# Performance work log

Measured on AMD Instinct MI355X. Metric: run time of the kernel, lower is better.

The kernel has to match this reference:

```python
import jax, jax.numpy as jnp
import numpy as np

B, T = 64, 4096
K = 67            # 25 body + 21 + 21 hand keypoints
D = 256           # first_layer_size
C = 7             # num_classes
THR = 0.1         # confidence_threshold
EPS = 1e-5        # BatchNorm eps


def setup_inputs() -> dict:
    key = jax.random.key(0)
    ks = jax.random.split(key, 8)
    body = jax.random.normal(ks[0], (B, T, 75), dtype=jnp.float32)
    hand_right = jax.random.normal(ks[1], (B, T, 63), dtype=jnp.float32)
    hand_left = jax.random.normal(ks[2], (B, T, 63), dtype=jnp.float32)
    length = jax.random.randint(ks[3], (B,), 1, T + 1, dtype=jnp.int64)
    W1 = jax.random.normal(ks[4], (2 * K, D), dtype=jnp.float32) * 0.05
    b1 = jnp.zeros((D,), dtype=jnp.float32)
    gamma = jnp.ones((D,), dtype=jnp.float32)
    beta = jnp.zeros((D,), dtype=jnp.float32)
    Wc = jax.random.normal(ks[5], (D, C), dtype=jnp.float32) * 0.05
    bc = jnp.zeros((C,), dtype=jnp.float32)
    return {"body": body, "hand_right": hand_right, "hand_left": hand_left,
            "length": length, "W1": W1, "b1": b1, "gamma": gamma,
            "beta": beta, "Wc": Wc, "bc": bc}


def reference(body, hand_right, hand_left, length, W1, b1, gamma, beta, Wc, bc):
    # concat keypoint streams -> [B, T, 3K] -> [B, T, K, 3]
    feats = jnp.concatenate([body, hand_right, hand_left], axis=2)
    feats = feats.reshape(feats.shape[0], feats.shape[1], -1, 3)
    x, y, conf = feats[..., 0], feats[..., 1], feats[..., 2]
    conf = (conf > THR).astype(feats.dtype)
    # gate coords by confidence, flatten to [B, T, 2K]
    pos = jnp.stack([x * conf, y * conf], axis=3)
    pos = pos.reshape(pos.shape[0], pos.shape[1], -1)
    # static MLP: Linear + ReLU -> [B, T, D]
    sf = jax.nn.relu(jnp.einsum("btf,fd->btd", pos, W1) + b1)
    # masked max pool over valid timesteps (vectorized segment-max)
    mask = jnp.arange(sf.shape[1])[None, :] < length[:, None]      # [B, T]
    pooled = jnp.max(jnp.where(mask[:, :, None], sf, -jnp.inf), axis=1)  # [B, D]
    # BatchNorm1d (training mode: batch statistics)
    mean = pooled.mean(axis=0)
    var = pooled.var(axis=0)
    bn = (pooled - mean) / jnp.sqrt(var + EPS) * gamma + beta
    # classifier
    return bn @ Wc + bc
```

## Files before the change

### kernel.cpp

```cpp
#include <hip/hip_runtime.h>
#include <hip/hip_bf16.h>

#define B_   64
#define T_   4096
#define K_   67
#define F_   134
#define FP_  160
#define D_   256
#define C_   7
#define THR_ 0.1f
#define EPS_ 1e-5f

typedef __bf16 bf16x8 __attribute__((ext_vector_type(8)));
typedef float  f32x4  __attribute__((ext_vector_type(4)));


__device__ __forceinline__ int a_idx(int t, int f) {
    return (((t >> 4) * 5 + (f >> 5)) * 512) +
           ((((f >> 3) & 3) * 16 + (t & 15)) * 8) + (f & 7);
}

__device__ __forceinline__ int get_len(const int* L, int b) {
    return (L[1] == 0) ? L[2 * b] : L[b];
}

__global__ void convert_w1(const float* __restrict__ W1, __bf16* __restrict__ W1bf) {
    int idx = blockIdx.x * 256 + threadIdx.x;
    if (idx >= D_ * FP_) return;
    int d = idx / FP_, f = idx - d * FP_;
    float v = (f < F_) ? W1[f * D_ + d] : 0.f;
    W1bf[idx] = (__bf16)v;
}

__device__ __forceinline__ void stage_triple(const float* p, int t, int kglob,
                                             __bf16* As) {
    float x = p[0], y = p[1], cf = p[2];
    if (!(cf > THR_)) { x = 0.f; y = 0.f; }
    unsigned short ux = __builtin_bit_cast(unsigned short, (__bf16)x);
    unsigned short uy = __builtin_bit_cast(unsigned short, (__bf16)y);
    int idx = a_idx(t, 2 * kglob);
    *(unsigned int*)((unsigned short*)As + idx) =
        (unsigned int)ux | ((unsigned int)uy << 16);
}

__global__ __launch_bounds__(256, 2)
void fused_mlp_pool(const float* __restrict__ body,
                    const float* __restrict__ hr,
                    const float* __restrict__ hl,
                    const int*   __restrict__ length,
                    const float* __restrict__ b1,
                    const __bf16* __restrict__ W1bf,
                    float* __restrict__ pooled)
{
    const int b = blockIdx.y;
    const int len = get_len(length, b);
    const int t0 = blockIdx.x * 64;
    if (t0 >= len) return;

    __shared__ __align__(16) __bf16 As[4 * 5 * 512];

    const int tid  = threadIdx.x;
    const int wave = tid >> 6;
    const int lane = tid & 63;
    const int quad = lane >> 4;
    const int l16  = lane & 15;
    const int dbase = wave * 64;

    bf16x8 bfrag[4][5];
    float  b1v[4];
#pragma unroll
    for (int n = 0; n < 4; n++) {
        int d = dbase + n * 16 + l16;
        const __bf16* p = W1bf + d * FP_ + quad * 8;
#pragma unroll
        for (int kt = 0; kt < 5; kt++)
            bfrag[n][kt] = *(const bf16x8*)(p + kt * 32);
        b1v[n] = b1[d];
    }

    for (int i = tid; i < 64 * 13; i += 256) {
        int t = i / 13;
        int f = 134 + 2 * (i % 13);
        *(unsigned int*)((unsigned short*)As + a_idx(t, f)) = 0u;
    }

    const long rowb = (long)b * T_;
    const float* bodyt = body + (rowb + t0) * 75;
    for (int j = tid; j < 64 * 25; j += 256) {
        int t = j / 25, k = j - t * 25;
        stage_triple(bodyt + t * 75 + k * 3, t, k, As);
    }
    const float* hrt = hr + (rowb + t0) * 63;
    for (int j = tid; j < 64 * 21; j += 256) {
        int t = j / 21, k = j - t * 21;
        stage_triple(hrt + t * 63 + k * 3, t, 25 + k, As);
    }
    const float* hlt = hl + (rowb + t0) * 63;
    for (int j = tid; j < 64 * 21; j += 256) {
        int t = j / 21, k = j - t * 21;
        stage_triple(hlt + t * 63 + k * 3, t, 46 + k, As);
    }
    __syncthreads();

    f32x4 acc[4][4];
#pragma unroll
    for (int m = 0; m < 4; m++)
#pragma unroll
        for (int n = 0; n < 4; n++)
            acc[m][n] = (f32x4){0.f, 0.f, 0.f, 0.f};

#pragma unroll
    for (int kt = 0; kt < 5; kt++) {
#pragma unroll
        for (int m = 0; m < 4; m++) {
            bf16x8 a = *(const bf16x8*)(As + (m * 5 + kt) * 512 + lane * 8);
#pragma unroll
            for (int n = 0; n < 4; n++)
                acc[m][n] = __builtin_amdgcn_mfma_f32_16x16x32_bf16(a, bfrag[n][kt], acc[m][n], 0, 0, 0);
        }
    }

    float runmax[4] = {0.f, 0.f, 0.f, 0.f};
#pragma unroll
    for (int m = 0; m < 4; m++) {
        int trow0 = t0 + m * 16 + quad * 4;
#pragma unroll
        for (int r = 0; r < 4; r++) {
            bool valid = (trow0 + r) < len;
#pragma unroll
            for (int n = 0; n < 4; n++) {
                float v = acc[m][n][r] + b1v[n];
                v = (v > 0.f) ? v : 0.f;
                runmax[n] = (valid && v > runmax[n]) ? v : runmax[n];
            }
        }
    }

#pragma unroll
    for (int n = 0; n < 4; n++) {
        float r = runmax[n];
        r = fmaxf(r, __shfl_xor(r, 16, 64));
        r = fmaxf(r, __shfl_xor(r, 32, 64));
        if (quad == n) {
            atomicMax((unsigned int*)(pooled + b * D_ + dbase + n * 16 + l16),
                      __float_as_uint(r));
        }
    }
}

__global__ void bn_classifier(const float* __restrict__ pooled,
                              const float* __restrict__ gamma,
                              const float* __restrict__ beta,
                              const float* __restrict__ Wc,
                              const float* __restrict__ bc,
                              float* __restrict__ out)
{
    __shared__ float scale_s[D_], shift_s[D_];
    const int tid = threadIdx.x;
    float s = 0.f, ss = 0.f;
#pragma unroll 8
    for (int b = 0; b < B_; b++) {
        float v = pooled[b * D_ + tid];
        s += v; ss += v * v;
    }
    float mean = s * (1.f / B_);
    float var  = ss * (1.f / B_) - mean * mean;
    var = fmaxf(var, 0.f);
    float sc = gamma[tid] * rsqrtf(var + EPS_);
    scale_s[tid] = sc;
    shift_s[tid] = beta[tid] - mean * sc;

    const int wv = tid >> 6, ln = tid & 63;
    float wcr[4][C_];
#pragma unroll
    for (int j = 0; j < 4; j++)
#pragma unroll
        for (int c = 0; c < C_; c++)
            wcr[j][c] = Wc[(ln * 4 + j) * C_ + c];
    __syncthreads();

    for (int b = wv * 16; b < wv * 16 + 16; b++) {
        float4 v = *(const float4*)(pooled + b * D_ + ln * 4);
        float q[4];
        q[0] = v.x * scale_s[ln * 4 + 0] + shift_s[ln * 4 + 0];
        q[1] = v.y * scale_s[ln * 4 + 1] + shift_s[ln * 4 + 1];
        q[2] = v.z * scale_s[ln * 4 + 2] + shift_s[ln * 4 + 2];
        q[3] = v.w * scale_s[ln * 4 + 3] + shift_s[ln * 4 + 3];
        float p[C_];
#pragma unroll
        for (int c = 0; c < C_; c++) p[c] = 0.f;
#pragma unroll
        for (int j = 0; j < 4; j++)
#pragma unroll
            for (int c = 0; c < C_; c++)
                p[c] += q[j] * wcr[j][c];
#pragma unroll
        for (int c = 0; c < C_; c++) {
#pragma unroll
            for (int off = 1; off < 64; off <<= 1)
                p[c] += __shfl_xor(p[c], off, 64);
        }
        if (ln == 0) {
#pragma unroll
            for (int c = 0; c < C_; c++)
                out[b * C_ + c] = p[c] + bc[c];
        }
    }
}

extern "C" void kernel_launch(void* const* d_in, const int* in_sizes, int n_in,
                              void* d_out, int out_size, void* d_ws, size_t ws_size,
                              hipStream_t stream) {
    const float* body   = (const float*)d_in[0];
    const float* hr     = (const float*)d_in[1];
    const float* hl     = (const float*)d_in[2];
    const int*   length = (const int*)  d_in[3];
    const float* W1     = (const float*)d_in[4];
    const float* b1     = (const float*)d_in[5];
    const float* gamma  = (const float*)d_in[6];
    const float* beta   = (const float*)d_in[7];
    const float* Wc     = (const float*)d_in[8];
    const float* bc     = (const float*)d_in[9];
    float* out = (float*)d_out;

    float*  pooled = (float*)d_ws;
    __bf16* W1bf   = (__bf16*)((char*)d_ws + 65536);

    hipMemsetAsync(d_ws, 0, 65536, stream);
    convert_w1<<<dim3(160), dim3(256), 0, stream>>>(W1, W1bf);
    fused_mlp_pool<<<dim3(64, B_), dim3(256), 0, stream>>>(body, hr, hl, length, b1, W1bf, pooled);
    bn_classifier<<<dim3(1), dim3(256), 0, stream>>>(pooled, gamma, beta, Wc, bc, out);
}
```

Measured before the change: 256.4 us.

## Stage keypoint rows via coalesced global_load_lds and halve the time tile

The fused MLP+pool kernel now copies the contiguous raw float rows for each block's time slice straight into LDS with global_load_lds. It then gates them and packs them to bf16 from LDS, instead of doing strided 3-float global reads per keypoint. The time tile drops from 64 to 32 rows, doubling the grid, and occupancy is hinted at 3 blocks per SM. The W1 conversion now uses a shared-memory transpose tile so its reads are coalesced. In exchange there is more LDS use, an extra barrier, and the W1 fragments and bias are reloaded across twice as many blocks.

Result: faster. 235.9 us (-8.0%).

```diff
diff --git a/kernel.cpp b/kernel.cpp
--- a/kernel.cpp
+++ b/kernel.cpp
@@ -14,36 +14,32 @@
 typedef __bf16 bf16x8 __attribute__((ext_vector_type(8)));
 typedef float  f32x4  __attribute__((ext_vector_type(4)));
 
-
-__device__ __forceinline__ int a_idx(int t, int f) {
-    return (((t >> 4) * 5 + (f >> 5)) * 512) +
-           ((((f >> 3) & 3) * 16 + (t & 15)) * 8) + (f & 7);
-}
+typedef __attribute__((address_space(1))) const unsigned int guint;
+typedef __attribute__((address_space(3))) unsigned int luint;
+
 
 __device__ __forceinline__ int get_len(const int* L, int b) {
     return (L[1] == 0) ? L[2 * b] : L[b];
 }
 
 __global__ void convert_w1(const float* __restrict__ W1, __bf16* __restrict__ W1bf) {
-    int idx = blockIdx.x * 256 + threadIdx.x;
-    if (idx >= D_ * FP_) return;
-    int d = idx / FP_, f = idx - d * FP_;
-    float v = (f < F_) ? W1[f * D_ + d] : 0.f;
-    W1bf[idx] = (__bf16)v;
-}
-
-__device__ __forceinline__ void stage_triple(const float* p, int t, int kglob,
-                                             __bf16* As) {
-    float x = p[0], y = p[1], cf = p[2];
-    if (!(cf > THR_)) { x = 0.f; y = 0.f; }
-    unsigned short ux = __builtin_bit_cast(unsigned short, (__bf16)x);
-    unsigned short uy = __builtin_bit_cast(unsigned short, (__bf16)y);
-    int idx = a_idx(t, 2 * kglob);
-    *(unsigned int*)((unsigned short*)As + idx) =
-        (unsigned int)ux | ((unsigned int)uy << 16);
-}
-
-__global__ __launch_bounds__(256, 2)
+    __shared__ float tile[32][33];
+    const int d0 = blockIdx.x * 32, f0 = blockIdx.y * 32;
+    const int tx = threadIdx.x & 31, ty = threadIdx.x >> 5;
+#pragma unroll
+    for (int r = 0; r < 32; r += 8) {
+        int f = f0 + ty + r;
+        tile[ty + r][tx] = (f < F_) ? W1[f * D_ + d0 + tx] : 0.f;
+    }
+    __syncthreads();
+#pragma unroll
+    for (int r = 0; r < 32; r += 8) {
+        int d = d0 + ty + r;
+        W1bf[d * FP_ + f0 + tx] = (__bf16)tile[tx][ty + r];
+    }
+}
+
+__global__ __launch_bounds__(256, 3)
 void fused_mlp_pool(const float* __restrict__ body,
                     const float* __restrict__ hr,
                     const float* __restrict__ hl,
@@ -54,10 +50,11 @@
 {
     const int b = blockIdx.y;
     const int len = get_len(length, b);
-    const int t0 = blockIdx.x * 64;
+    const int t0 = blockIdx.x * 32;
     if (t0 >= len) return;
 
-    __shared__ __align__(16) __bf16 As[4 * 5 * 512];
+    __shared__ __align__(16) float  raw[6432];
+    __shared__ __align__(16) __bf16 As[10 * 512];
 
     const int tid  = threadIdx.x;
     const int wave = tid >> 6;
@@ -66,6 +63,32 @@
     const int l16  = lane & 15;
     const int dbase = wave * 64;
 
+    const long rowb = (long)b * T_;
+    const float* bodyt = body + (rowb + t0) * 75;
+    const float* hrt   = hr   + (rowb + t0) * 63;
+    const float* hlt   = hl   + (rowb + t0) * 63;
+
+    for (int i = wave; i < 9; i += 4)
+        __builtin_amdgcn_global_load_lds(
+            (guint*)(bodyt + i * 256 + lane * 4),
+            (luint*)((char*)raw + i * 1024 + lane * 16), 16, 0, 0);
+    for (int i = wave; i < 7; i += 4)
+        __builtin_amdgcn_global_load_lds(
+            (guint*)(hrt + i * 256 + lane * 4),
+            (luint*)((char*)raw + 9600 + i * 1024 + lane * 16), 16, 0, 0);
+    for (int i = wave; i < 7; i += 4)
+        __builtin_amdgcn_global_load_lds(
+            (guint*)(hlt + i * 256 + lane * 4),
+            (luint*)((char*)raw + 17664 + i * 1024 + lane * 16), 16, 0, 0);
+
+    if (tid < 136) {
+        const float* g; int loff;
+        if (tid < 24)      { g = bodyt + 2304 + tid * 4;        loff = 2304 + tid * 4; }
+        else if (tid < 80) { g = hrt + 1792 + (tid - 24) * 4;   loff = 4192 + (tid - 24) * 4; }
+        else               { g = hlt + 1792 + (tid - 80) * 4;   loff = 6208 + (tid - 80) * 4; }
+        *(float4*)(raw + loff) = *(const float4*)g;
+    }
+
     bf16x8 bfrag[4][5];
     float  b1v[4];
 #pragma unroll
@@ -78,33 +101,44 @@
         b1v[n] = b1[d];
     }
 
-    for (int i = tid; i < 64 * 13; i += 256) {
-        int t = i / 13;
-        int f = 134 + 2 * (i % 13);
-        *(unsigned int*)((unsigned short*)As + a_idx(t, f)) = 0u;
-    }
-
-    const long rowb = (long)b * T_;
-    const float* bodyt = body + (rowb + t0) * 75;
-    for (int j = tid; j < 64 * 25; j += 256) {
-        int t = j / 25, k = j - t * 25;
-        stage_triple(bodyt + t * 75 + k * 3, t, k, As);
-    }
-    const float* hrt = hr + (rowb + t0) * 63;
-    for (int j = tid; j < 64 * 21; j += 256) {
-        int t = j / 21, k = j - t * 21;
-        stage_triple(hrt + t * 63 + k * 3, t, 25 + k, As);
-    }
-    const float* hlt = hl + (rowb + t0) * 63;
-    for (int j = tid; j < 64 * 21; j += 256) {
-        int t = j / 21, k = j - t * 21;
-        stage_triple(hlt + t * 63 + k * 3, t, 46 + k, As);
-    }
-    __syncthreads();
-
-    f32x4 acc[4][4];
-#pragma unroll
-    for (int m = 0; m < 4; m++)
+    for (int i = tid; i < 416; i += 256) {
+        int t = i & 31, kp = 67 + (i >> 5);
+        int w = ((t >> 4) * 5 + (kp >> 4)) * 256 + (((kp >> 2) & 3) * 16 + (t & 15)) * 4 + (kp & 3);
+        ((unsigned int*)As)[w] = 0u;
+    }
+    __syncthreads();
+
+#pragma unroll
+    for (int it = 0; it < 8; it++) {
+        int idx = it * 256 + tid;
+        int t = (((idx >> 5) & 3) << 3) | ((idx >> 2) & 7);
+        int k = (((idx >> 7) & 15) << 2) | (idx & 3);
+        int roff;
+        if (k < 25)      roff = t * 75 + 3 * k;
+        else if (k < 46) roff = 2400 + t * 63 + 3 * (k - 25);
+        else             roff = 4416 + t * 63 + 3 * (k - 46);
+        float x = raw[roff], y = raw[roff + 1], cf = raw[roff + 2];
+        if (!(cf > THR_)) { x = 0.f; y = 0.f; }
+        unsigned short ux = __builtin_bit_cast(unsigned short, (__bf16)x);
+        unsigned short uy = __builtin_bit_cast(unsigned short, (__bf16)y);
+        int w = ((t >> 4) * 5 + (k >> 4)) * 256 + (((k >> 2) & 3) * 16 + (t & 15)) * 4 + (k & 3);
+        ((unsigned int*)As)[w] = (unsigned int)ux | ((unsigned int)uy << 16);
+    }
+    if (tid < 96) {
+        int t = tid & 31, k = 64 + (tid >> 5);
+        int roff = 4416 + t * 63 + 3 * (k - 46);
+        float x = raw[roff], y = raw[roff + 1], cf = raw[roff + 2];
+        if (!(cf > THR_)) { x = 0.f; y = 0.f; }
+        unsigned short ux = __builtin_bit_cast(unsigned short, (__bf16)x);
+        unsigned short uy = __builtin_bit_cast(unsigned short, (__bf16)y);
+        int w = ((t >> 4) * 5 + (k >> 4)) * 256 + (((k >> 2) & 3) * 16 + (t & 15)) * 4 + (k & 3);
+        ((unsigned int*)As)[w] = (unsigned int)ux | ((unsigned int)uy << 16);
+    }
+    __syncthreads();
+
+    f32x4 acc[2][4];
+#pragma unroll
+    for (int m = 0; m < 2; m++)
 #pragma unroll
         for (int n = 0; n < 4; n++)
             acc[m][n] = (f32x4){0.f, 0.f, 0.f, 0.f};
@@ -112,7 +146,7 @@
 #pragma unroll
     for (int kt = 0; kt < 5; kt++) {
 #pragma unroll
-        for (int m = 0; m < 4; m++) {
+        for (int m = 0; m < 2; m++) {
             bf16x8 a = *(const bf16x8*)(As + (m * 5 + kt) * 512 + lane * 8);
 #pragma unroll
             for (int n = 0; n < 4; n++)
@@ -122,7 +156,7 @@
 
     float runmax[4] = {0.f, 0.f, 0.f, 0.f};
 #pragma unroll
-    for (int m = 0; m < 4; m++) {
+    for (int m = 0; m < 2; m++) {
         int trow0 = t0 + m * 16 + quad * 4;
 #pragma unroll
         for (int r = 0; r < 4; r++) {
@@ -135,7 +169,6 @@
             }
         }
     }
-
 #pragma unroll
     for (int n = 0; n < 4; n++) {
         float r = runmax[n];
@@ -227,7 +260,7 @@
     __bf16* W1bf   = (__bf16*)((char*)d_ws + 65536);
 
     hipMemsetAsync(d_ws, 0, 65536, stream);
-    convert_w1<<<dim3(160), dim3(256), 0, stream>>>(W1, W1bf);
-    fused_mlp_pool<<<dim3(64, B_), dim3(256), 0, stream>>>(body, hr, hl, length, b1, W1bf, pooled);
+    convert_w1<<<dim3(8, 5), dim3(256), 0, stream>>>(W1, W1bf);
+    fused_mlp_pool<<<dim3(128, B_), dim3(256), 0, stream>>>(body, hr, hl, length, b1, W1bf, pooled);
     bn_classifier<<<dim3(1), dim3(256), 0, stream>>>(pooled, gamma, beta, Wc, bc, out);
 }
```
